# Kernel optimization log

Hardware: AMD Instinct MI355X
Metric: run time of the kernel (lower is better)

Reference implementation:

```python
import jax, jax.numpy as jnp
import numpy as np

N_NODES = 100000
N_EDGES = 3200000
IN_FEATS = 512
N_HIDDEN = 256
N_CLASSES = 64
K_STEPS = 10
ALPHA = 0.2


def setup_inputs() -> dict:
    key = jax.random.key(0)
    ks = jax.random.split(key, 8)
    x = jax.random.normal(ks[0], (N_NODES, IN_FEATS), dtype=jnp.float32)
    edge_index = jax.random.randint(ks[1], (2, N_EDGES), 0, N_NODES, dtype=jnp.int64)
    # Glorot-ish scaled weights for the 3-layer MLP: in->hidden, hidden->hidden... wait n_layers=3 -> in->hid, hid->hid, hid->classes
    W0 = jax.random.normal(ks[2], (IN_FEATS, N_HIDDEN), dtype=jnp.float32) * (1.0 / np.sqrt(IN_FEATS))
    b0 = jnp.zeros((N_HIDDEN,), dtype=jnp.float32)
    W1 = jax.random.normal(ks[3], (N_HIDDEN, N_HIDDEN), dtype=jnp.float32) * (1.0 / np.sqrt(N_HIDDEN))
    b1 = jnp.zeros((N_HIDDEN,), dtype=jnp.float32)
    W2 = jax.random.normal(ks[4], (N_HIDDEN, N_CLASSES), dtype=jnp.float32) * (1.0 / np.sqrt(N_HIDDEN))
    b2 = jnp.zeros((N_CLASSES,), dtype=jnp.float32)
    return {"x": x, "edge_index": edge_index, "W0": W0, "b0": b0, "W1": W1, "b1": b1, "W2": W2, "b2": b2}


def reference(x, edge_index, W0, b0, W1, b1, W2, b2):
    N = x.shape[0]
    # MLP stack (eval mode: dropout is identity)
    h = jax.nn.relu(x @ W0 + b0)
    h = jax.nn.relu(h @ W1 + b1)
    h = h @ W2 + b2  # [N, C]

    # GCN normalization with self-loops (PyG APPNP default)
    loop = jnp.arange(N, dtype=edge_index.dtype)
    row = jnp.concatenate([edge_index[0], loop])  # source
    col = jnp.concatenate([edge_index[1], loop])  # target
    deg = jax.ops.segment_sum(jnp.ones_like(col, dtype=h.dtype), col, num_segments=N)
    deg_inv_sqrt = jnp.where(deg > 0, jax.lax.rsqrt(deg), 0.0)
    norm = deg_inv_sqrt[row] * deg_inv_sqrt[col]  # [E+N]

    # APPNP propagation: z_{k+1} = (1-alpha) * A_hat z_k + alpha * h
    def step(z, _):
        msg = norm[:, None] * z[row]  # gather over sources
        agg = jax.ops.segment_sum(msg, col, num_segments=N)  # scatter to targets
        return (1.0 - ALPHA) * agg + ALPHA * h, None

    z, _ = jax.lax.scan(step, h, None, length=K_STEPS)
    return z
```

## Files before the change

### kernel.cpp

```cpp
#include <hip/hip_runtime.h>
#include <cstdint>
#include <cstddef>

#define NN 100000
#define BSHIFT 9
#define NBUK ((NN + 511) >> 9)
#define NB_PART 256
#define PART_T 256

typedef __attribute__((ext_vector_type(4))) float f32x4;
typedef __attribute__((ext_vector_type(8))) short bf16x8;
typedef __attribute__((ext_vector_type(8))) _Float16 f16x8;

__device__ __forceinline__ unsigned short f2bf(float x) {
    unsigned int u = __builtin_bit_cast(unsigned int, x);
    unsigned int r = (u + 0x7fffu + ((u >> 16) & 1u)) >> 16;
    return (unsigned short)r;
}

__global__ void dis_kernel(const int* __restrict__ cnt, float* __restrict__ dis, int N) {
    int i = blockIdx.x * blockDim.x + threadIdx.x;
    if (i < N) dis[i] = rsqrtf((float)(cnt[i] + 1));
}

#define SCAN_B 128
#define SCAN_T 256
#define SCAN_CH 4

__global__ __launch_bounds__(SCAN_T) void scan_part_kernel(const int* __restrict__ cnt,
                                                           int* __restrict__ bsum, int N) {
    __shared__ int s[SCAN_T];
    int b = blockIdx.x, t = threadIdx.x;
    int base = b * SCAN_T * SCAN_CH + t * SCAN_CH;
    int sum = 0;
#pragma unroll
    for (int j = 0; j < SCAN_CH; ++j) {
        int i = base + j;
        if (i < N) sum += cnt[i];
    }
    s[t] = sum;
    __syncthreads();
    for (int off = SCAN_T / 2; off > 0; off >>= 1) {
        if (t < off) s[t] += s[t + off];
        __syncthreads();
    }
    if (t == 0) bsum[b] = s[0];
}

__global__ __launch_bounds__(SCAN_B) void scan_bsum_kernel(const int* __restrict__ bsum,
                                                           int* __restrict__ bofs) {
    __shared__ int s[SCAN_B];
    int t = threadIdx.x;
    int v = bsum[t];
    s[t] = v;
    __syncthreads();
    for (int off = 1; off < SCAN_B; off <<= 1) {
        int x = (t >= off) ? s[t - off] : 0;
        __syncthreads();
        s[t] += x;
        __syncthreads();
    }
    bofs[t] = s[t] - v;
}

__global__ __launch_bounds__(SCAN_T) void scan_write_kernel(const int* __restrict__ cnt,
                                                            const int* __restrict__ bofs,
                                                            int* __restrict__ rowptr,
                                                            int N, int E) {
    __shared__ int s[SCAN_T];
    int b = blockIdx.x, t = threadIdx.x;
    int base = b * SCAN_T * SCAN_CH + t * SCAN_CH;
    int loc[SCAN_CH];
    int sum = 0;
#pragma unroll
    for (int j = 0; j < SCAN_CH; ++j) {
        int i = base + j;
        int c = (i < N) ? cnt[i] : 0;
        loc[j] = c;
        sum += c;
    }
    s[t] = sum;
    __syncthreads();
    for (int off = 1; off < SCAN_T; off <<= 1) {
        int x = (t >= off) ? s[t - off] : 0;
        __syncthreads();
        s[t] += x;
        __syncthreads();
    }
    int run = bofs[b] + s[t] - sum;
#pragma unroll
    for (int j = 0; j < SCAN_CH; ++j) {
        int i = base + j;
        if (i < N) {
            rowptr[i] = run;
            run += loc[j];
        }
    }
    if (b == 0 && t == 0) rowptr[N] = E;
}

__global__ __launch_bounds__(PART_T) void part_count_kernel(const int* __restrict__ ecol,
                                                            int* __restrict__ blockcnt, int E) {
    __shared__ int hist[NBUK];
    int b = blockIdx.x, t = threadIdx.x;
    for (int i = t; i < NBUK; i += PART_T) hist[i] = 0;
    __syncthreads();
    int CH = (E + NB_PART - 1) / NB_PART;
    int lo = b * CH;
    int hi = lo + CH; if (hi > E) hi = E;
    for (int e = lo + t; e < hi; e += PART_T)
        atomicAdd(&hist[ecol[e] >> BSHIFT], 1);
    __syncthreads();
    for (int i = t; i < NBUK; i += PART_T) blockcnt[i * NB_PART + b] = hist[i];
}

__global__ __launch_bounds__(NB_PART) void part_scan_kernel(const int* __restrict__ blockcnt,
                                                            int* __restrict__ boffrel,
                                                            int* __restrict__ buktot) {
    __shared__ int s[NB_PART];
    int k = blockIdx.x, t = threadIdx.x;
    int v = blockcnt[k * NB_PART + t];
    s[t] = v;
    __syncthreads();
    for (int off = 1; off < NB_PART; off <<= 1) {
        int x = (t >= off) ? s[t - off] : 0;
        __syncthreads();
        s[t] += x;
        __syncthreads();
    }
    boffrel[k * NB_PART + t] = s[t] - v;
    if (t == NB_PART - 1) buktot[k] = s[t];
}

__global__ __launch_bounds__(256) void buk_scan_kernel(const int* __restrict__ buktot,
                                                       int* __restrict__ bukbase) {
    __shared__ int s[256];
    int t = threadIdx.x;
    int v = (t < NBUK) ? buktot[t] : 0;
    s[t] = v;
    __syncthreads();
    for (int off = 1; off < 256; off <<= 1) {
        int x = (t >= off) ? s[t - off] : 0;
        __syncthreads();
        s[t] += x;
        __syncthreads();
    }
    if (t < NBUK) bukbase[t] = s[t] - v;
}

__global__ __launch_bounds__(PART_T) void part_write_kernel(const int* __restrict__ erow,
                                                            const int* __restrict__ ecol,
                                                            const int* __restrict__ boffrel,
                                                            const int* __restrict__ bukbase,
                                                            unsigned int* __restrict__ staging, int E) {
    __shared__ int lofs[NBUK];
    int b = blockIdx.x, t = threadIdx.x;
    for (int i = t; i < NBUK; i += PART_T) lofs[i] = bukbase[i] + boffrel[i * NB_PART + b];
    __syncthreads();
    int CH = (E + NB_PART - 1) / NB_PART;
    int lo = b * CH;
    int hi = lo + CH; if (hi > E) hi = E;
    for (int e = lo + t; e < hi; e += PART_T) {
        int c = ecol[e], r = erow[e];
        int k = c >> BSHIFT;
        int pos = atomicAdd(&lofs[k], 1);
        staging[pos] = (unsigned)r | ((unsigned)(c & 511) << 20);
    }
}

__global__ __launch_bounds__(512) void buk_nodecount_kernel(const unsigned int* __restrict__ staging,
                                                            const int* __restrict__ bukbase,
                                                            const int* __restrict__ buktot,
                                                            int* __restrict__ cnt, int N) {
    __shared__ int hist[512];
    int k = blockIdx.x, t = threadIdx.x;
    hist[t] = 0;
    __syncthreads();
    int lo = bukbase[k];
    int hi = lo + buktot[k];
    for (int e = lo + t; e < hi; e += 512)
        atomicAdd(&hist[staging[e] >> 20], 1);
    __syncthreads();
    int node = (k << BSHIFT) + t;
    if (node < N) cnt[node] = hist[t];
}

__global__ __launch_bounds__(512) void part_scatter_kernel(const unsigned int* __restrict__ staging,
                                                           const int* __restrict__ rowptr,
                                                           int* __restrict__ srcs, int N, int E) {
    __shared__ int lnxt[512];
    int k = blockIdx.x, t = threadIdx.x;
    int base = k << BSHIFT;
    int node = base + t;
    lnxt[t] = (node < N) ? rowptr[node] : 0;
    __syncthreads();
    int estart = rowptr[base];
    int hiidx = base + 512; if (hiidx > N) hiidx = N;
    int eend = rowptr[hiidx];
    for (int e = estart + t; e < eend; e += 512) {
        unsigned v = staging[e];
        int p = atomicAdd(&lnxt[v >> 20], 1);
        srcs[p] = (int)(v & 0xFFFFFu);
    }
}

__global__ void cvt_bf16_kernel(const float* __restrict__ in, unsigned short* __restrict__ out,
                                size_t n) {
    size_t i = ((size_t)blockIdx.x * blockDim.x + threadIdx.x) * 8;
    size_t stride = (size_t)gridDim.x * blockDim.x * 8;
    for (; i < n; i += stride) {
        float4 a = *(const float4*)(in + i);
        float4 b = *(const float4*)(in + i + 4);
        union { unsigned short u[8]; uint4 v; } r;
        r.u[0] = f2bf(a.x); r.u[1] = f2bf(a.y); r.u[2] = f2bf(a.z); r.u[3] = f2bf(a.w);
        r.u[4] = f2bf(b.x); r.u[5] = f2bf(b.y); r.u[6] = f2bf(b.z); r.u[7] = f2bf(b.w);
        *(uint4*)(out + i) = r.v;
    }
}

__global__ void wt_cvt_kernel(const float* __restrict__ W, unsigned short* __restrict__ Wt,
                              int K, int N, int Npad) {
    int idx = blockIdx.x * blockDim.x + threadIdx.x;
    int total = Npad * K;
    if (idx >= total) return;
    int n = idx / K, k = idx - n * K;
    float v = (n < N) ? W[(size_t)k * N + n] : 0.f;
    Wt[idx] = f2bf(v);
}

template <int RELU, int FINAL>
__global__ __launch_bounds__(256) void gemm_mfma_kernel(
    const unsigned short* __restrict__ A, const unsigned short* __restrict__ Bt,
    const float* __restrict__ bias, unsigned short* __restrict__ Cb,
    _Float16* __restrict__ h16out, _Float16* __restrict__ u16out, const float* __restrict__ dis,
    int M, int K, int N) {
    __shared__ unsigned short sA[128 * 64];
    __shared__ unsigned short sB[128 * 64];
    const int t = threadIdx.x;
    const int wid = t >> 6, lane = t & 63;
    const int bm = blockIdx.x * 128, bn = blockIdx.y * 128;
    const int wr = wid >> 1, wc = wid & 1;

    const int srow = lane >> 3;
    const int skb = (lane & 7) * 8;

    f32x4 acc[4][4] = {};

    for (int k0 = 0; k0 < K; k0 += 64) {
#pragma unroll
        for (int j = 0; j < 4; ++j) {
            int rbase = (wid * 4 + j) * 8;
            int grow = bm + rbase + srow;
            if (grow >= M) grow = M - 1;
            const unsigned short* asrc = A + (size_t)grow * K + k0 + skb;
            __builtin_amdgcn_global_load_lds(
                (const __attribute__((address_space(1))) unsigned int*)asrc,
                (__attribute__((address_space(3))) unsigned int*)&sA[rbase * 64], 16, 0, 0);
            int gcol = bn + rbase + srow;
            const unsigned short* bsrc = Bt + (size_t)gcol * K + k0 + skb;
            __builtin_amdgcn_global_load_lds(
                (const __attribute__((address_space(1))) unsigned int*)bsrc,
                (__attribute__((address_space(3))) unsigned int*)&sB[rbase * 64], 16, 0, 0);
        }
        __syncthreads();

        const int fr = lane & 15;
        const int fk = (lane >> 4) * 8;
#pragma unroll
        for (int ks = 0; ks < 2; ++ks) {
            bf16x8 af[4], bfr[4];
#pragma unroll
            for (int m = 0; m < 4; ++m)
                af[m] = *(const bf16x8*)&sA[(wr * 64 + m * 16 + fr) * 64 + ks * 32 + fk];
#pragma unroll
            for (int n = 0; n < 4; ++n)
                bfr[n] = *(const bf16x8*)&sB[(wc * 64 + n * 16 + fr) * 64 + ks * 32 + fk];
#pragma unroll
            for (int m = 0; m < 4; ++m)
#pragma unroll
                for (int n = 0; n < 4; ++n)
                    acc[m][n] = __builtin_amdgcn_mfma_f32_16x16x32_bf16(af[m], bfr[n], acc[m][n], 0, 0, 0);
        }
        __syncthreads();
    }

    const int fr = lane & 15, fq = (lane >> 4) * 4;
#pragma unroll
    for (int m = 0; m < 4; ++m) {
#pragma unroll
        for (int n = 0; n < 4; ++n) {
            int col = bn + wc * 64 + n * 16 + fr;
            if (col >= N) continue;
            float bv = bias[col];
#pragma unroll
            for (int q = 0; q < 4; ++q) {
                int r = bm + wr * 64 + m * 16 + fq + q;
                if (r >= M) continue;
                float v = acc[m][n][q] + bv;
                if (RELU) v = fmaxf(v, 0.f);
                if (!FINAL) {
                    Cb[(size_t)r * N + col] = f2bf(v);
                } else {
                    h16out[(size_t)r * 64 + col] = (_Float16)v;
                    u16out[(size_t)r * 64 + col] = (_Float16)(dis[r] * v);
                }
            }
        }
    }
}

template <int RELU>
__global__ __launch_bounds__(256) void gemm_bias_kernel(
    const float* __restrict__ A, const float* __restrict__ B,
    const float* __restrict__ bias, float* __restrict__ C,
    int M, int K, int N) {
    __shared__ float sA[16][64];
    __shared__ float sB[16][64];
    const int bm = blockIdx.x * 64;
    const int bn = blockIdx.y * 64;
    const int t = threadIdx.x;
    const int tx = t & 15, ty = t >> 4;
    const int arow_l = t >> 2;
    const int akk = (t & 3) * 4;
    const int brow = t >> 4;
    const int bcol = (t & 15) * 4;
    float acc[4][4] = {};

    for (int k0 = 0; k0 < K; k0 += 16) {
        float4 av = make_float4(0.f, 0.f, 0.f, 0.f);
        int arow = bm + arow_l;
        if (arow < M) av = *(const float4*)(A + (size_t)arow * K + k0 + akk);
        float4 bv = *(const float4*)(B + (size_t)(k0 + brow) * N + bn + bcol);
        sA[akk + 0][arow_l] = av.x;
        sA[akk + 1][arow_l] = av.y;
        sA[akk + 2][arow_l] = av.z;
        sA[akk + 3][arow_l] = av.w;
        *(float4*)&sB[brow][bcol] = bv;
        __syncthreads();
#pragma unroll
        for (int k = 0; k < 16; ++k) {
            float4 a4 = *(const float4*)&sA[k][ty * 4];
            float4 b4 = *(const float4*)&sB[k][tx * 4];
            acc[0][0] += a4.x * b4.x; acc[0][1] += a4.x * b4.y; acc[0][2] += a4.x * b4.z; acc[0][3] += a4.x * b4.w;
            acc[1][0] += a4.y * b4.x; acc[1][1] += a4.y * b4.y; acc[1][2] += a4.y * b4.z; acc[1][3] += a4.y * b4.w;
            acc[2][0] += a4.z * b4.x; acc[2][1] += a4.z * b4.y; acc[2][2] += a4.z * b4.z; acc[2][3] += a4.z * b4.w;
            acc[3][0] += a4.w * b4.x; acc[3][1] += a4.w * b4.y; acc[3][2] += a4.w * b4.z; acc[3][3] += a4.w * b4.w;
        }
        __syncthreads();
    }

#pragma unroll
    for (int i = 0; i < 4; ++i) {
        int row = bm + ty * 4 + i;
        if (row >= M) continue;
#pragma unroll
        for (int j = 0; j < 4; ++j) {
            int colg = bn + tx * 4 + j;
            float v = acc[i][j] + bias[colg];
            if (RELU) v = fmaxf(v, 0.f);
            C[(size_t)row * N + colg] = v;
        }
    }
}

__global__ void h16u0_kernel(const float* __restrict__ h, const float* __restrict__ dis,
                             _Float16* __restrict__ h16, _Float16* __restrict__ u16, int total) {
    int i = blockIdx.x * blockDim.x + threadIdx.x;
    if (i < total) {
        float v = h[i];
        h16[i] = (_Float16)v;
        u16[i] = (_Float16)(dis[i >> 6] * v);
    }
}

template <int FINAL>
__global__ __launch_bounds__(256) void appnp_step16_kernel(
    const int* __restrict__ rowptr, const int* __restrict__ srcs,
    const float* __restrict__ dis, const _Float16* __restrict__ uin,
    const _Float16* __restrict__ hbuf, void* __restrict__ outbuf, int N) {
    int node = blockIdx.x * 4 + (threadIdx.x >> 6);
    if (node >= N) return;
    int lane = threadIdx.x & 63;
    int eg = lane >> 3;
    int fl = lane & 7;

    int start = rowptr[node];
    int end = rowptr[node + 1];
    float acc[8] = {};
    for (int e = start + eg; e < end; e += 8) {
        int s = srcs[e];
        f16x8 zv = *(const f16x8*)(uin + (size_t)s * 64 + fl * 8);
#pragma unroll
        for (int j = 0; j < 8; ++j) acc[j] += (float)zv[j];
    }
#pragma unroll
    for (int j = 0; j < 8; ++j) {
        acc[j] += __shfl_xor(acc[j], 8);
        acc[j] += __shfl_xor(acc[j], 16);
        acc[j] += __shfl_xor(acc[j], 32);
    }

    if (eg == 0) {
        float d = dis[node];
        f16x8 us = *(const f16x8*)(uin + (size_t)node * 64 + fl * 8);
        f16x8 hv = *(const f16x8*)(hbuf + (size_t)node * 64 + fl * 8);
        float o[8];
#pragma unroll
        for (int j = 0; j < 8; ++j)
            o[j] = 0.8f * d * (acc[j] + (float)us[j]) + 0.2f * (float)hv[j];
        if (FINAL) {
            float* op = (float*)outbuf + (size_t)node * 64 + fl * 8;
            float4 o0 = make_float4(o[0], o[1], o[2], o[3]);
            float4 o1 = make_float4(o[4], o[5], o[6], o[7]);
            *(float4*)op = o0;
            *(float4*)(op + 4) = o1;
        } else {
            f16x8 ov;
#pragma unroll
            for (int j = 0; j < 8; ++j) ov[j] = (_Float16)(d * o[j]);
            *(f16x8*)((_Float16*)outbuf + (size_t)node * 64 + fl * 8) = ov;
        }
    }
}

extern "C" void kernel_launch(void* const* d_in, const int* in_sizes, int n_in,
                              void* d_out, int out_size, void* d_ws, size_t ws_size,
                              hipStream_t stream) {
    const float* x  = (const float*)d_in[0];
    const int*   ei = (const int*)d_in[1];
    const float* W0 = (const float*)d_in[2];
    const float* b0 = (const float*)d_in[3];
    const float* W1 = (const float*)d_in[4];
    const float* b1 = (const float*)d_in[5];
    const float* W2 = (const float*)d_in[6];
    const float* b2 = (const float*)d_in[7];
    float* out = (float*)d_out;

    const int N = NN;
    const int E = in_sizes[1] / 2;
    const int* erow = ei;
    const int* ecol = ei + E;
    (void)out_size; (void)n_in;

    char* ws = (char*)d_ws;
    size_t off = 0;
    auto alloc = [&](size_t bytes) -> void* {
        void* p = ws + off;
        off += (bytes + 255) & ~(size_t)255;
        return p;
    };
    int*   cnt      = (int*)alloc((size_t)N * 4);
    int*   rowptr   = (int*)alloc((size_t)(N + 1) * 4);
    float* dis      = (float*)alloc((size_t)N * 4);
    int*   bsum     = (int*)alloc((size_t)SCAN_B * 4);
    int*   bofs     = (int*)alloc((size_t)SCAN_B * 4);
    int*   blockcnt = (int*)alloc((size_t)NBUK * NB_PART * 4);
    int*   boffrel  = (int*)alloc((size_t)NBUK * NB_PART * 4);
    int*   buktot   = (int*)alloc((size_t)NBUK * 4);
    int*   bukbase  = (int*)alloc((size_t)NBUK * 4);
    unsigned int* staging = (unsigned int*)alloc((size_t)E * 4);
    int*   srcs     = (int*)alloc((size_t)E * 4);
    _Float16* h16 = (_Float16*)alloc((size_t)N * 64 * 2);
    _Float16* ua  = (_Float16*)alloc((size_t)N * 64 * 2);
    _Float16* ub  = (_Float16*)alloc((size_t)N * 64 * 2);
    size_t common_end = off;

    size_t need_bf16 = common_end
        + (((size_t)N * 512 * 2 + 255) & ~(size_t)255)
        + ((256 * 512 * 2 + 255) & ~(size_t)255)
        + ((256 * 256 * 2 + 255) & ~(size_t)255)
        + ((128 * 256 * 2 + 255) & ~(size_t)255)
        + (((size_t)N * 256 * 2 + 255) & ~(size_t)255)
        + (((size_t)N * 256 * 2 + 255) & ~(size_t)255);
    const bool use_bf16 = (ws_size >= need_bf16 + (1u << 20));

    part_count_kernel<<<NB_PART, PART_T, 0, stream>>>(ecol, blockcnt, E);
    part_scan_kernel<<<NBUK, NB_PART, 0, stream>>>(blockcnt, boffrel, buktot);
    buk_scan_kernel<<<1, 256, 0, stream>>>(buktot, bukbase);
    part_write_kernel<<<NB_PART, PART_T, 0, stream>>>(erow, ecol, boffrel, bukbase, staging, E);
    buk_nodecount_kernel<<<NBUK, 512, 0, stream>>>(staging, bukbase, buktot, cnt, N);
    dis_kernel<<<(N + 255) / 256, 256, 0, stream>>>(cnt, dis, N);
    scan_part_kernel<<<SCAN_B, SCAN_T, 0, stream>>>(cnt, bsum, N);
    scan_bsum_kernel<<<1, SCAN_B, 0, stream>>>(bsum, bofs);
    scan_write_kernel<<<SCAN_B, SCAN_T, 0, stream>>>(cnt, bofs, rowptr, N, E);
    part_scatter_kernel<<<NBUK, 512, 0, stream>>>(staging, rowptr, srcs, N, E);

    if (use_bf16) {
        unsigned short* xb  = (unsigned short*)alloc((size_t)N * 512 * 2);
        unsigned short* Wt0 = (unsigned short*)alloc(256 * 512 * 2);
        unsigned short* Wt1 = (unsigned short*)alloc(256 * 256 * 2);
        unsigned short* Wt2 = (unsigned short*)alloc(128 * 256 * 2);
        unsigned short* h1b = (unsigned short*)alloc((size_t)N * 256 * 2);
        unsigned short* h2b = (unsigned short*)alloc((size_t)N * 256 * 2);

        cvt_bf16_kernel<<<2048, 256, 0, stream>>>(x, xb, (size_t)N * 512);
        wt_cvt_kernel<<<(256 * 512 + 255) / 256, 256, 0, stream>>>(W0, Wt0, 512, 256, 256);
        wt_cvt_kernel<<<(256 * 256 + 255) / 256, 256, 0, stream>>>(W1, Wt1, 256, 256, 256);
        wt_cvt_kernel<<<(128 * 256 + 255) / 256, 256, 0, stream>>>(W2, Wt2, 256, 64, 128);

        const int gm = (N + 127) / 128;
        dim3 g0(gm, 2);
        gemm_mfma_kernel<1, 0><<<g0, 256, 0, stream>>>(xb, Wt0, b0, h1b, nullptr, nullptr, nullptr, N, 512, 256);
        gemm_mfma_kernel<1, 0><<<g0, 256, 0, stream>>>(h1b, Wt1, b1, h2b, nullptr, nullptr, nullptr, N, 256, 256);
        dim3 g2(gm, 1);
        gemm_mfma_kernel<0, 1><<<g2, 256, 0, stream>>>(h2b, Wt2, b2, nullptr, h16, ua, dis, N, 256, 64);
    } else {
        const int Ms = 12500;
        float* hf  = (float*)alloc((size_t)N * 64 * 4);
        float* h1s = (float*)alloc((size_t)Ms * 256 * 4);
        float* h2s = (float*)alloc((size_t)Ms * 256 * 4);
        for (int s0 = 0; s0 < N; s0 += Ms) {
            int rows = (N - s0 < Ms) ? (N - s0) : Ms;
            dim3 g1((rows + 63) / 64, 4);
            gemm_bias_kernel<1><<<g1, 256, 0, stream>>>(x + (size_t)s0 * 512, W0, b0, h1s, rows, 512, 256);
            gemm_bias_kernel<1><<<g1, 256, 0, stream>>>(h1s, W1, b1, h2s, rows, 256, 256);
            dim3 g3((rows + 63) / 64, 1);
            gemm_bias_kernel<0><<<g3, 256, 0, stream>>>(h2s, W2, b2, hf + (size_t)s0 * 64, rows, 256, 64);
        }
        h16u0_kernel<<<(N * 64 + 255) / 256, 256, 0, stream>>>(hf, dis, h16, ua, N * 64);
    }

    const _Float16* uin = ua;
    for (int k = 0; k < 10; ++k) {
        if (k == 9) {
            appnp_step16_kernel<1><<<(N + 3) / 4, 256, 0, stream>>>(rowptr, srcs, dis, uin, h16, out, N);
        } else {
            _Float16* uout = (k & 1) ? ua : ub;
            appnp_step16_kernel<0><<<(N + 3) / 4, 256, 0, stream>>>(rowptr, srcs, dis, uin, h16, uout, N);
            uin = uout;
        }
    }
}
```

Before: 1.018 ms.

## Split propagation features into 16-wide chunks with chunk-major layout for cache locality

Stores h and u in a [chunk][node][16] half layout and runs the APPNP step over 4 feature chunks sequentially, with each wave handling one node-chunk using 32 edges in parallel. This shrinks the random-gather working set per chunk so it stays cache resident, reducing DRAM traffic from scattered row gathers. In exchange, the CSR source indices are read four times per step, more shuffle reductions are needed, and each gather is only 32 bytes.

Result: slower. 1.988 ms (+95.3%).

```diff
diff --git a/kernel.cpp b/kernel.cpp
--- a/kernel.cpp
+++ b/kernel.cpp
@@ -301,8 +301,9 @@
                 if (!FINAL) {
                     Cb[(size_t)r * N + col] = f2bf(v);
                 } else {
-                    h16out[(size_t)r * 64 + col] = (_Float16)v;
-                    u16out[(size_t)r * 64 + col] = (_Float16)(dis[r] * v);
+                    size_t idx = (size_t)(col >> 4) * ((size_t)M * 16) + (size_t)r * 16 + (col & 15);
+                    h16out[idx] = (_Float16)v;
+                    u16out[idx] = (_Float16)(dis[r] * v);
                 }
             }
         }
@@ -367,34 +368,40 @@
                              _Float16* __restrict__ h16, _Float16* __restrict__ u16, int total) {
     int i = blockIdx.x * blockDim.x + threadIdx.x;
     if (i < total) {
+        int r = i >> 6, col = i & 63;
         float v = h[i];
-        h16[i] = (_Float16)v;
-        u16[i] = (_Float16)(dis[i >> 6] * v);
+        size_t idx = (size_t)(col >> 4) * ((size_t)NN * 16) + (size_t)r * 16 + (col & 15);
+        h16[idx] = (_Float16)v;
+        u16[idx] = (_Float16)(dis[r] * v);
     }
 }
 
 template <int FINAL>
-__global__ __launch_bounds__(256) void appnp_step16_kernel(
+__global__ __launch_bounds__(256) void appnp_chunk16_kernel(
     const int* __restrict__ rowptr, const int* __restrict__ srcs,
     const float* __restrict__ dis, const _Float16* __restrict__ uin,
-    const _Float16* __restrict__ hbuf, void* __restrict__ outbuf, int N) {
-    int node = blockIdx.x * 4 + (threadIdx.x >> 6);
-    if (node >= N) return;
+    const _Float16* __restrict__ hbuf, void* __restrict__ outbuf) {
+    int unit = blockIdx.x * 4 + (threadIdx.x >> 6);
+    int chunk = unit / NN;
+    int node = unit - chunk * NN;
     int lane = threadIdx.x & 63;
-    int eg = lane >> 3;
-    int fl = lane & 7;
-
+    int eg = lane >> 1;
+    int fl = lane & 1;
+
+    const _Float16* up = uin + (size_t)chunk * (NN * 16);
     int start = rowptr[node];
     int end = rowptr[node + 1];
     float acc[8] = {};
-    for (int e = start + eg; e < end; e += 8) {
+    for (int e = start + eg; e < end; e += 32) {
         int s = srcs[e];
-        f16x8 zv = *(const f16x8*)(uin + (size_t)s * 64 + fl * 8);
+        f16x8 zv = *(const f16x8*)(up + s * 16 + fl * 8);
 #pragma unroll
         for (int j = 0; j < 8; ++j) acc[j] += (float)zv[j];
     }
 #pragma unroll
     for (int j = 0; j < 8; ++j) {
+        acc[j] += __shfl_xor(acc[j], 2);
+        acc[j] += __shfl_xor(acc[j], 4);
         acc[j] += __shfl_xor(acc[j], 8);
         acc[j] += __shfl_xor(acc[j], 16);
         acc[j] += __shfl_xor(acc[j], 32);
@@ -402,23 +409,21 @@
 
     if (eg == 0) {
         float d = dis[node];
-        f16x8 us = *(const f16x8*)(uin + (size_t)node * 64 + fl * 8);
-        f16x8 hv = *(const f16x8*)(hbuf + (size_t)node * 64 + fl * 8);
+        f16x8 us = *(const f16x8*)(up + node * 16 + fl * 8);
+        f16x8 hv = *(const f16x8*)(hbuf + (size_t)chunk * (NN * 16) + node * 16 + fl * 8);
         float o[8];
 #pragma unroll
         for (int j = 0; j < 8; ++j)
             o[j] = 0.8f * d * (acc[j] + (float)us[j]) + 0.2f * (float)hv[j];
         if (FINAL) {
-            float* op = (float*)outbuf + (size_t)node * 64 + fl * 8;
-            float4 o0 = make_float4(o[0], o[1], o[2], o[3]);
-            float4 o1 = make_float4(o[4], o[5], o[6], o[7]);
-            *(float4*)op = o0;
-            *(float4*)(op + 4) = o1;
+            float* op = (float*)outbuf + (size_t)node * 64 + chunk * 16 + fl * 8;
+            *(float4*)op = make_float4(o[0], o[1], o[2], o[3]);
+            *(float4*)(op + 4) = make_float4(o[4], o[5], o[6], o[7]);
         } else {
             f16x8 ov;
 #pragma unroll
             for (int j = 0; j < 8; ++j) ov[j] = (_Float16)(d * o[j]);
-            *(f16x8*)((_Float16*)outbuf + (size_t)node * 64 + fl * 8) = ov;
+            *(f16x8*)((_Float16*)outbuf + (size_t)chunk * (NN * 16) + node * 16 + fl * 8) = ov;
         }
     }
 }
@@ -523,10 +528,10 @@
     const _Float16* uin = ua;
     for (int k = 0; k < 10; ++k) {
         if (k == 9) {
-            appnp_step16_kernel<1><<<(N + 3) / 4, 256, 0, stream>>>(rowptr, srcs, dis, uin, h16, out, N);
+            appnp_chunk16_kernel<1><<<N, 256, 0, stream>>>(rowptr, srcs, dis, uin, h16, out);
         } else {
             _Float16* uout = (k & 1) ? ua : ub;
-            appnp_step16_kernel<0><<<(N + 3) / 4, 256, 0, stream>>>(rowptr, srcs, dis, uin, h16, uout, N);
+            appnp_chunk16_kernel<0><<<N, 256, 0, stream>>>(rowptr, srcs, dis, uin, h16, uout);
             uin = uout;
         }
     }
```
